# Performance work log

Hardware: AMD Instinct MI355X
Metric: run time of the kernel (lower is better)

Reference implementation:

```python
import jax, jax.numpy as jnp
import numpy as np

FIRE_RATE = 0.5
ANGLE = 0.0


def _kernels(angle):
    dx = np.outer([1, 2, 1], [-1, 0, 1]) / 8.0
    dy = dx.T
    dlap = np.array([[1, 2, 1], [2, -12, 2], [1, 2, 1]]) / 8.0
    dlap2 = np.array([[0, 1, 0], [1, -4, 1], [0, 1, 0]]) / 8.0
    c = np.cos(angle * np.pi / 180.0)
    s = np.sin(angle * np.pi / 180.0)
    w1 = c * dx - s * dy
    w2 = s * dx + c * dy
    return [jnp.asarray(k, jnp.float32) for k in (w1, w2, dlap, dlap2)]


def _dwconv(x, k):
    # x: [B,H,W,C], k: [3,3] applied depthwise (same kernel every channel)
    C = x.shape[-1]
    rhs = jnp.broadcast_to(k[:, :, None, None], (3, 3, 1, C))
    return jax.lax.conv_general_dilated(
        x, rhs, window_strides=(1, 1), padding='SAME',
        dimension_numbers=('NHWC', 'HWIO', 'NHWC'), feature_group_count=C)


def _alive(x):
    # 3x3 max-pool (stride 1, SAME) over alpha channel (index 3) > 0.1
    a = jax.lax.reduce_window(x[..., 3:4], -jnp.inf, jax.lax.max,
                              (1, 3, 3, 1), (1, 1, 1, 1), 'SAME')
    return a > 0.1


def _update(x, W0, b0, W1, key):
    pre_life = _alive(x)                                  # [B,H,W,1] bool
    ks = _kernels(ANGLE)
    y = jnp.concatenate([x] + [_dwconv(x, k) for k in ks], axis=-1)  # [B,H,W,5C]
    h = jax.nn.relu(y @ W0 + b0)                          # [B,H,W,hidden]
    d = h @ W1                                            # [B,H,W,C]
    stoch = (jax.random.uniform(key, d.shape[:3] + (1,)) > FIRE_RATE).astype(d.dtype)
    x = x + d * stoch
    life = (pre_life & _alive(x)).astype(x.dtype)
    return x * life


def setup_inputs() -> dict:
    key = jax.random.key(0)
    k1, k2, k3, k4 = jax.random.split(key, 4)
    B, H, W, C, HID = 8, 256, 256, 16, 128
    return {
        'x': jax.random.normal(k1, (B, H, W, C), jnp.float32),
        'W0': jax.random.normal(k2, (5 * C, HID), jnp.float32) * 0.05,
        'b0': jax.random.normal(k3, (HID,), jnp.float32) * 0.05,
        'W1': jax.random.normal(k4, (HID, C), jnp.float32) * 0.05,
        'steps': 2,
    }


def reference(x, W0, b0, W1, steps):
    base = jax.random.key(42)
    for step in range(steps):
        x = _update(x, W0, b0, W1, jax.random.fold_in(base, step))
    return x
```

## Files before the change

### kernel.cpp

```cpp
#include <hip/hip_runtime.h>
#include <stdint.h>

#define BB 8
#define HH 256
#define WW 256
#define CC 16
#define HID 128
#define NPIX (BB*HH*WW)
#define MTILE 64
#define NBLK (NPIX/MTILE)

typedef _Float16 h8 __attribute__((ext_vector_type(8)));
typedef __fp16   fp16v2 __attribute__((ext_vector_type(2)));
typedef float    f4 __attribute__((ext_vector_type(4)));

#define YPK_HI     0
#define YPK_MID    3328
#define ALPHA5_OFF 6656
#define LIFE_OFF   6996
#define LDS_DW     8192

__host__ __device__ __forceinline__ uint32_t rotl32(uint32_t x, int r) {
  return (x << r) | (x >> (32 - r));
}

__host__ __device__ inline void threefry2x32(uint32_t k0, uint32_t k1,
                                             uint32_t x0, uint32_t x1,
                                             uint32_t& o0, uint32_t& o1) {
  const uint32_t ks2 = k0 ^ k1 ^ 0x1BD11BDAu;
  x0 += k0; x1 += k1;
#define TF_R4(a,b,c,d) \
  x0 += x1; x1 = rotl32(x1,(a)); x1 ^= x0; \
  x0 += x1; x1 = rotl32(x1,(b)); x1 ^= x0; \
  x0 += x1; x1 = rotl32(x1,(c)); x1 ^= x0; \
  x0 += x1; x1 = rotl32(x1,(d)); x1 ^= x0;
  TF_R4(13,15,26,6)   x0 += k1;  x1 += ks2 + 1u;
  TF_R4(17,29,16,24)  x0 += ks2; x1 += k0 + 2u;
  TF_R4(13,15,26,6)   x0 += k0;  x1 += k1 + 3u;
  TF_R4(17,29,16,24)  x0 += k1;  x1 += ks2 + 4u;
  TF_R4(13,15,26,6)   x0 += ks2; x1 += k0 + 5u;
#undef TF_R4
  o0 = x0; o1 = x1;
}

__device__ __forceinline__ void split2(float a, float b, uint32_t& hi, uint32_t& mid) {
  _Float16 ha = (_Float16)a, hb = (_Float16)b;
  union { _Float16 h[2]; uint32_t u; } ph;
  ph.h[0] = ha; ph.h[1] = hb; hi = ph.u;
  float ra = a - (float)ha, rb = b - (float)hb;
  union { fp16v2 h; uint32_t u; } pu;
  pu.h = __builtin_amdgcn_cvt_pkrtz(ra, rb);
  mid = pu.u;
}

__global__ __launch_bounds__(256)
void prep_frags(const float* __restrict__ W0g, const float* __restrict__ W1g,
                uint32_t* __restrict__ W0F, uint32_t* __restrict__ W1F) {
  const int tid = blockIdx.x * 256 + threadIdx.x;
  for (int idx = tid; idx < 6144; idx += gridDim.x * 256) {
    const int r = idx & 3, l = (idx >> 2) & 63, ks = (idx >> 8) % 3, n = idx / 768;
    const int g = l >> 4, c = l & 15;
    const int k0 = 32 * ks + 8 * g + 2 * r;
    const int hid = 16 * n + c;
    const float a = (k0     < 80) ? W0g[k0 * HID + hid]       : 0.f;
    const float b = (k0 + 1 < 80) ? W0g[(k0 + 1) * HID + hid] : 0.f;
    uint32_t hi, mid; split2(a, b, hi, mid);
    W0F[(size_t)(((n * 3 + ks) * 2 + 0) * 64 + l) * 4 + r] = hi;
    W0F[(size_t)(((n * 3 + ks) * 2 + 1) * 64 + l) * 4 + r] = mid;
  }
  for (int idx = tid; idx < 1024; idx += gridDim.x * 256) {
    const int r = idx & 3, l = (idx >> 2) & 63, ks = idx >> 8;
    const int g = l >> 4, c = l & 15;
    float va[2];
#pragma unroll
    for (int h = 0; h < 2; ++h) {
      const int khat = 2 * g + 16 * (r & 1) + 8 * h + (r >> 1);
      va[h] = W1g[(size_t)(32 * ks + khat) * CC + c];
    }
    uint32_t hi, mid; split2(va[0], va[1], hi, mid);
    W1F[(size_t)((ks * 2 + 0) * 64 + l) * 4 + r] = hi;
    W1F[(size_t)((ks * 2 + 1) * 64 + l) * 4 + r] = mid;
  }
}

template <int APPLY_LIFE>
__global__ __launch_bounds__(256, 5)
void step_fused(const float* __restrict__ xin,
                const uint32_t* __restrict__ W0F,
                const uint32_t* __restrict__ W1F,
                const float* __restrict__ b0g,
                const float* __restrict__ aPrev,
                const unsigned char* __restrict__ mPrev,
                float* __restrict__ xn,
                float* __restrict__ alpha_out,
                unsigned char* __restrict__ prelife,
                uint32_t k0, uint32_t k1) {
  __shared__ uint32_t LDSU[LDS_DW];
  float* const LDSF = (float*)LDSU;

  const int t    = threadIdx.x;
  const int blk  = blockIdx.x;
  const int lane = t & 63;
  const int w    = __builtin_amdgcn_readfirstlane(t >> 6);
  const int g    = lane >> 4;
  const int c15  = lane & 15;

  uint4 BH[2][2], BM[2][2];
#pragma unroll
  for (int nl = 0; nl < 2; ++nl) {
    const int n = 2 * w + nl;
    BH[0][nl] = *(const uint4*)(W0F + (size_t)(((n * 3 + 0) * 2 + 0) * 64 + lane) * 4);
    BM[0][nl] = *(const uint4*)(W0F + (size_t)(((n * 3 + 0) * 2 + 1) * 64 + lane) * 4);
  }
  const float bv0 = b0g[16 * (2 * w + 0) + c15];
  const float bv1 = b0g[16 * (2 * w + 1) + c15];

  const int base_ = blk * MTILE;
  const int bi    = base_ >> 16;
  const int rc    = base_ & 0xFFFF;
  const int ic    = rc >> 8;
  const int jc0   = rc & 0xFF;

  if constexpr (APPLY_LIFE) {
    const float* ap = aPrev + (size_t)bi * (HH * WW);
    for (int it = t; it < 340; it += 256) {
      const int r = it / 68, c = it - r * 68;
      const int ii = ic - 2 + r, jj = jc0 - 2 + c;
      float v = 0.f;
      if ((unsigned)ii < (unsigned)HH && (unsigned)jj < (unsigned)WW)
        v = ap[ii * WW + jj];
      LDSF[ALPHA5_OFF + it] = v;
    }
    __syncthreads();
    if (t < 198) {
      const int r = t / 66, xx = t - r * 66;
      const float* a0 = &LDSF[ALPHA5_OFF + r * 68 + xx];
      const float m0 = fmaxf(fmaxf(a0[0],   a0[1]),   a0[2]);
      const float m1 = fmaxf(fmaxf(a0[68],  a0[69]),  a0[70]);
      const float m2 = fmaxf(fmaxf(a0[136], a0[137]), a0[138]);
      const float mm = fmaxf(fmaxf(m0, m1), m2);
      const int ii = ic - 1 + r, jj = jc0 - 1 + xx;
      int pl = 0;
      if ((unsigned)ii < (unsigned)HH && (unsigned)jj < (unsigned)WW)
        pl = mPrev[(size_t)bi * (HH * WW) + ii * WW + jj];
      LDSF[LIFE_OFF + t] = (pl && mm > 0.1f) ? 1.0f : 0.0f;
    }
    __syncthreads();
  }

  const int px  = 16 * w + c15;
  const int c4  = 4 * g;
  const int gpx = base_ + px;
  const int jc  = jc0 + px;

  const float DXW[3][3] = {{-0.125f, 0.0f, 0.125f},
                           {-0.25f,  0.0f, 0.25f },
                           {-0.125f, 0.0f, 0.125f}};
  const float DYW[3][3] = {{-0.125f, -0.25f, -0.125f},
                           { 0.0f,    0.0f,   0.0f  },
                           { 0.125f,  0.25f,  0.125f}};
  const float LPW[3][3] = {{0.125f, 0.25f, 0.125f},
                           {0.25f, -1.5f,  0.25f },
                           {0.125f, 0.25f, 0.125f}};
  const float L2W[3][3] = {{0.0f,   0.125f, 0.0f  },
                           {0.125f, -0.5f,  0.125f},
                           {0.0f,   0.125f, 0.0f  }};

  float ctr[4] = {0,0,0,0};
  float adx[4] = {0,0,0,0};
  float ady[4] = {0,0,0,0};
  float alp[4] = {0,0,0,0};
  float al2[4] = {0,0,0,0};
  float amax = 0.0f;

  const float* xb = xin + (size_t)bi * (HH * WW * CC);
#pragma unroll
  for (int di = -1; di <= 1; ++di) {
#pragma unroll
    for (int dj = -1; dj <= 1; ++dj) {
      const int ii = ic + di, jj = jc + dj;
      const bool ok = ((unsigned)ii < (unsigned)HH) && ((unsigned)jj < (unsigned)WW);
      float4 p = make_float4(0.f, 0.f, 0.f, 0.f);
      if (ok) p = *(const float4*)(xb + ((size_t)(ii * WW + jj) * CC + c4));
      if constexpr (APPLY_LIFE) {
        const float lf = LDSF[LIFE_OFF + (di + 1) * 66 + (px + dj + 1)];
        p.x *= lf; p.y *= lf; p.z *= lf; p.w *= lf;
      }
      const float wdx = DXW[di+1][dj+1], wdy = DYW[di+1][dj+1];
      const float wlp = LPW[di+1][dj+1], wl2 = L2W[di+1][dj+1];
      const float pv[4] = {p.x, p.y, p.z, p.w};
#pragma unroll
      for (int q = 0; q < 4; ++q) {
        if (di == 0 && dj == 0) ctr[q] = pv[q];
        if (wdx != 0.f) adx[q] = fmaf(pv[q], wdx, adx[q]);
        if (wdy != 0.f) ady[q] = fmaf(pv[q], wdy, ady[q]);
        if (wlp != 0.f) alp[q] = fmaf(pv[q], wlp, alp[q]);
        if (wl2 != 0.f) al2[q] = fmaf(pv[q], wl2, al2[q]);
      }
      if (g == 0) amax = fmaxf(amax, p.w);
    }
  }

  float fire01;
  {
    uint32_t lo, hi2;
    threefry2x32(k0, k1, 0u, (uint32_t)gpx, lo, hi2);
    const uint32_t bits = lo ^ hi2;
    const float u = __uint_as_float((bits >> 9) | 0x3f800000u) - 1.0f;
    fire01 = (u > 0.5f) ? 1.0f : 0.0f;
  }

  {
    const int q2 = g << 1;
#define WRYPK(grp, A) do { \
    uint32_t h0_, m0_, h1_, m1_; \
    split2(A[0], A[1], h0_, m0_); split2(A[2], A[3], h1_, m1_); \
    const int kk_ = 8 * (grp) + q2; \
    *(uint2*)&LDSU[YPK_HI  + px * 52 + kk_] = make_uint2(h0_, h1_); \
    *(uint2*)&LDSU[YPK_MID + px * 52 + kk_] = make_uint2(m0_, m1_); \
  } while (0)
    WRYPK(0, ctr); WRYPK(1, adx); WRYPK(2, ady); WRYPK(3, alp); WRYPK(4, al2);
#undef WRYPK
  }
#pragma unroll
  for (int j = 0; j < 4; ++j) {
    const int pos = t * 4 + j;
    const int plane = pos >> 9, rem = pos & 511;
    LDSU[plane * 3328 + (rem >> 3) * 52 + 40 + (rem & 7)] = 0u;
  }
  if (g == 0) prelife[gpx] = (amax > 0.1f) ? 1 : 0;

  __syncthreads();

  f4 C1[4][2];
#pragma unroll
  for (int m = 0; m < 4; ++m) {
    C1[m][0] = (f4){bv0, bv0, bv0, bv0};
    C1[m][1] = (f4){bv1, bv1, bv1, bv1};
  }

#define LOADB(par, kss) do { \
  _Pragma("unroll") for (int nl_ = 0; nl_ < 2; ++nl_) { \
    const int n_ = 2 * w + nl_; \
    BH[par][nl_] = *(const uint4*)(W0F + (size_t)(((n_ * 3 + (kss)) * 2 + 0) * 64 + lane) * 4); \
    BM[par][nl_] = *(const uint4*)(W0F + (size_t)(((n_ * 3 + (kss)) * 2 + 1) * 64 + lane) * 4); \
  } } while (0)

  const int abase = c15 * 52 + 4 * g;
#pragma unroll
  for (int ks = 0; ks < 3; ++ks) {
    if (ks == 0) LOADB(1, 1);
    if (ks == 1) LOADB(0, 2);
    const int cur = ks & 1;
#pragma unroll
    for (int m = 0; m < 4; ++m) {
      const uint4 uh = *(const uint4*)&LDSU[YPK_HI  + abase + m * 832 + 16 * ks];
      const uint4 um = *(const uint4*)&LDSU[YPK_MID + abase + m * 832 + 16 * ks];
      const h8 ah = __builtin_bit_cast(h8, uh);
      const h8 am = __builtin_bit_cast(h8, um);
#pragma unroll
      for (int nl = 0; nl < 2; ++nl) {
        const h8 bh = __builtin_bit_cast(h8, BH[cur][nl]);
        const h8 bm = __builtin_bit_cast(h8, BM[cur][nl]);
        C1[m][nl] = __builtin_amdgcn_mfma_f32_16x16x32_f16(ah, bh, C1[m][nl], 0, 0, 0);
        C1[m][nl] = __builtin_amdgcn_mfma_f32_16x16x32_f16(am, bh, C1[m][nl], 0, 0, 0);
        C1[m][nl] = __builtin_amdgcn_mfma_f32_16x16x32_f16(ah, bm, C1[m][nl], 0, 0, 0);
      }
    }
  }
#undef LOADB

  __syncthreads();

  {
    const int sg = (g & 1) << 4;
    const int hid0 = 32 * w + c15;
    const int hid1 = hid0 + 16;
    const int hx00 = hid0 ^ sg,       hx01 = hid0 ^ (sg | 1);
    const int hx02 = hid0 ^ (sg | 8), hx03 = hid0 ^ (sg | 9);
    const int hx10 = hid1 ^ sg,       hx11 = hid1 ^ (sg | 1);
    const int hx12 = hid1 ^ (sg | 8), hx13 = hid1 ^ (sg | 9);
#pragma unroll
    for (int m = 0; m < 4; ++m) {
      const int rowb = (16 * m + 4 * g) * 128;
      {
        f4 hv = C1[m][0];
        LDSF[rowb +   0 + hx00] = fmaxf(hv.x, 0.f);
        LDSF[rowb + 128 + hx01] = fmaxf(hv.y, 0.f);
        LDSF[rowb + 256 + hx02] = fmaxf(hv.z, 0.f);
        LDSF[rowb + 384 + hx03] = fmaxf(hv.w, 0.f);
      }
      {
        f4 hv = C1[m][1];
        LDSF[rowb +   0 + hx10] = fmaxf(hv.x, 0.f);
        LDSF[rowb + 128 + hx11] = fmaxf(hv.y, 0.f);
        LDSF[rowb + 256 + hx12] = fmaxf(hv.z, 0.f);
        LDSF[rowb + 384 + hx13] = fmaxf(hv.w, 0.f);
      }
    }
  }

  uint4 W1H[4], W1M[4];
#pragma unroll
  for (int ks = 0; ks < 4; ++ks) {
    W1H[ks] = *(const uint4*)(W1F + (size_t)((ks * 2 + 0) * 64 + lane) * 4);
    W1M[ks] = *(const uint4*)(W1F + (size_t)((ks * 2 + 1) * 64 + lane) * 4);
  }

  __syncthreads();

  f4 C2 = (f4){0.f, 0.f, 0.f, 0.f};
  {
    const int swzr  = (c15 & 1) | ((c15 & 6) << 2);
    const int hbase = px * 128 + 2 * g;
    int ka[4], kb[4];
#pragma unroll
    for (int r = 0; r < 4; ++r) {
      const int K0 = 16 * (r & 1) + (r >> 1);
      ka[r] = K0 ^ swzr;
      kb[r] = (K0 + 8) ^ swzr;
    }
#pragma unroll
    for (int ks = 0; ks < 4; ++ks) {
      uint32_t ph[4], pm[4];
#pragma unroll
      for (int r = 0; r < 4; ++r) {
        const float a = LDSF[hbase + 32 * ks + ka[r]];
        const float b = LDSF[hbase + 32 * ks + kb[r]];
        split2(a, b, ph[r], pm[r]);
      }
      const uint4 uh = make_uint4(ph[0], ph[1], ph[2], ph[3]);
      const uint4 um = make_uint4(pm[0], pm[1], pm[2], pm[3]);
      const h8 bh = __builtin_bit_cast(h8, uh);
      const h8 bm = __builtin_bit_cast(h8, um);
      const h8 ah = __builtin_bit_cast(h8, W1H[ks]);
      const h8 am = __builtin_bit_cast(h8, W1M[ks]);
      C2 = __builtin_amdgcn_mfma_f32_16x16x32_f16(ah, bh, C2, 0, 0, 0);
      C2 = __builtin_amdgcn_mfma_f32_16x16x32_f16(am, bh, C2, 0, 0, 0);
      C2 = __builtin_amdgcn_mfma_f32_16x16x32_f16(ah, bm, C2, 0, 0, 0);
    }
  }

  {
    f4 xv;
    xv.x = fmaf(C2.x, fire01, ctr[0]);
    xv.y = fmaf(C2.y, fire01, ctr[1]);
    xv.z = fmaf(C2.z, fire01, ctr[2]);
    xv.w = fmaf(C2.w, fire01, ctr[3]);
    *(f4*)&xn[(size_t)gpx * CC + c4] = xv;
    if (g == 0) alpha_out[gpx] = xv.w;
  }
}

__global__ __launch_bounds__(256)
void life_final(float* __restrict__ out,
                const float* __restrict__ alpha,
                const unsigned char* __restrict__ prelife) {
  const int idx = blockIdx.x * 256 + threadIdx.x;
  const int b  = idx >> 16;
  const int ij = idx & 0xFFFF;
  const int i  = ij >> 8;
  const int j  = ij & 0xFF;

  const float* ab = alpha + (size_t)b * (HH * WW);
  float amax = 0.0f;
#pragma unroll
  for (int di = -1; di <= 1; ++di) {
    const int ii = i + di;
    if ((unsigned)ii >= (unsigned)HH) continue;
#pragma unroll
    for (int dj = -1; dj <= 1; ++dj) {
      const int jj = j + dj;
      if ((unsigned)jj >= (unsigned)WW) continue;
      amax = fmaxf(amax, ab[(size_t)ii * WW + jj]);
    }
  }
  const bool life = (prelife[idx] != 0) && (amax > 0.1f);
  if (!life) {
    const float4 z = make_float4(0.0f, 0.0f, 0.0f, 0.0f);
    float4* dst = (float4*)(out + (size_t)idx * CC);
    dst[0] = z; dst[1] = z; dst[2] = z; dst[3] = z;
  }
}

extern "C" void kernel_launch(void* const* d_in, const int* in_sizes, int n_in,
                              void* d_out, int out_size, void* d_ws, size_t ws_size,
                              hipStream_t stream) {
  (void)in_sizes; (void)n_in; (void)out_size; (void)ws_size;
  const float* x  = (const float*)d_in[0];
  const float* W0 = (const float*)d_in[1];
  const float* b0 = (const float*)d_in[2];
  const float* W1 = (const float*)d_in[3];
  float* out = (float*)d_out;

  float* xn = (float*)d_ws;
  float* alphaA = xn + (size_t)NPIX * CC;
  float* alphaB = alphaA + NPIX;
  unsigned char* maskA = (unsigned char*)(alphaB + NPIX);
  unsigned char* maskB = maskA + NPIX;
  uint32_t* W0F = (uint32_t*)(maskB + NPIX);
  uint32_t* W1F = W0F + 12288;

  prep_frags<<<24, 256, 0, stream>>>(W0, W1, W0F, W1F);

  uint32_t fk0, fk1;
  threefry2x32(0u, 42u, 0u, 0u, fk0, fk1);
  step_fused<0><<<NBLK, 256, 0, stream>>>(x, W0F, W1F, b0, nullptr, nullptr,
                                          xn, alphaA, maskA, fk0, fk1);
  threefry2x32(0u, 42u, 0u, 1u, fk0, fk1);
  step_fused<1><<<NBLK, 256, 0, stream>>>(xn, W0F, W1F, b0, alphaA, maskA,
                                          out, alphaB, maskB, fk0, fk1);
  life_final<<<NPIX / 256, 256, 0, stream>>>(out, alphaB, maskB);
}
```

Measured before the change: 222.7 us.

## Fold depthwise stencils into W0 and feed raw 3x3 patches to MFMA

The four fixed 3x3 depthwise kernels and the identity channel are folded into the first layer's weights on the device, producing an effective 144x128 weight over the raw 3x3 neighbourhood. The main kernel now stages a 3x66 halo of the input into LDS once per block as split fp16 hi/mid values and feeds the 9 taps directly to the MFMAs. This replaces per-thread 9-tap global gathers and scalar stencil FMAs. In exchange, K grows from 96 to 160, so each block issues more MFMAs. The folded weights also change the rounding of the hi/mid split.

```diff
diff --git a/kernel.cpp b/kernel.cpp
--- a/kernel.cpp
+++ b/kernel.cpp
@@ -14,10 +14,12 @@
 typedef __fp16   fp16v2 __attribute__((ext_vector_type(2)));
 typedef float    f4 __attribute__((ext_vector_type(4)));
 
-#define YPK_HI     0
-#define YPK_MID    3328
-#define ALPHA5_OFF 6656
-#define LIFE_OFF   6996
+#define XH_OFF     0
+#define XM_OFF     2112
+#define ALF_OFF    4224
+#define ALPHA5_OFF 4424
+#define LIFE_OFF   4764
+#define HS_OFF     0
 #define LDS_DW     8192
 
 __host__ __device__ __forceinline__ uint32_t rotl32(uint32_t x, int r) {
@@ -56,17 +58,33 @@
 __global__ __launch_bounds__(256)
 void prep_frags(const float* __restrict__ W0g, const float* __restrict__ W1g,
                 uint32_t* __restrict__ W0F, uint32_t* __restrict__ W1F) {
+  const float KW[5][9] = {
+    {0.f,0.f,0.f, 0.f,1.f,0.f, 0.f,0.f,0.f},
+    {-0.125f,0.f,0.125f, -0.25f,0.f,0.25f, -0.125f,0.f,0.125f},
+    {-0.125f,-0.25f,-0.125f, 0.f,0.f,0.f, 0.125f,0.25f,0.125f},
+    {0.125f,0.25f,0.125f, 0.25f,-1.5f,0.25f, 0.125f,0.25f,0.125f},
+    {0.f,0.125f,0.f, 0.125f,-0.5f,0.125f, 0.f,0.125f,0.f}};
   const int tid = blockIdx.x * 256 + threadIdx.x;
-  for (int idx = tid; idx < 6144; idx += gridDim.x * 256) {
-    const int r = idx & 3, l = (idx >> 2) & 63, ks = (idx >> 8) % 3, n = idx / 768;
+  for (int idx = tid; idx < 10240; idx += gridDim.x * 256) {
+    const int r = idx & 3, l = (idx >> 2) & 63;
+    const int ks = (idx >> 8) % 5, n = (idx >> 8) / 5;
     const int g = l >> 4, c = l & 15;
-    const int k0 = 32 * ks + 8 * g + 2 * r;
     const int hid = 16 * n + c;
-    const float a = (k0     < 80) ? W0g[k0 * HID + hid]       : 0.f;
-    const float b = (k0 + 1 < 80) ? W0g[(k0 + 1) * HID + hid] : 0.f;
-    uint32_t hi, mid; split2(a, b, hi, mid);
-    W0F[(size_t)(((n * 3 + ks) * 2 + 0) * 64 + l) * 4 + r] = hi;
-    W0F[(size_t)(((n * 3 + ks) * 2 + 1) * 64 + l) * 4 + r] = mid;
+    float v[2];
+#pragma unroll
+    for (int h = 0; h < 2; ++h) {
+      const int k = 32 * ks + 8 * g + 2 * r + h;
+      float acc = 0.f;
+      if (k < 144) {
+        const int tap = k >> 4, ch = k & 15;
+        for (int grp = 0; grp < 5; ++grp)
+          acc += KW[grp][tap] * W0g[(16 * grp + ch) * HID + hid];
+      }
+      v[h] = acc;
+    }
+    uint32_t hi, mid; split2(v[0], v[1], hi, mid);
+    W0F[(size_t)(((n * 5 + ks) * 2 + 0) * 64 + l) * 4 + r] = hi;
+    W0F[(size_t)(((n * 5 + ks) * 2 + 1) * 64 + l) * 4 + r] = mid;
   }
   for (int idx = tid; idx < 1024; idx += gridDim.x * 256) {
     const int r = idx & 3, l = (idx >> 2) & 63, ks = idx >> 8;
@@ -106,12 +124,13 @@
   const int c15  = lane & 15;
 
   uint4 BH[2][2], BM[2][2];
-#pragma unroll
-  for (int nl = 0; nl < 2; ++nl) {
-    const int n = 2 * w + nl;
-    BH[0][nl] = *(const uint4*)(W0F + (size_t)(((n * 3 + 0) * 2 + 0) * 64 + lane) * 4);
-    BM[0][nl] = *(const uint4*)(W0F + (size_t)(((n * 3 + 0) * 2 + 1) * 64 + lane) * 4);
-  }
+#define LOADB(buf, kss) do { \
+  _Pragma("unroll") for (int nl_ = 0; nl_ < 2; ++nl_) { \
+    const int n_ = 2 * w + nl_; \
+    BH[buf][nl_] = *(const uint4*)(W0F + (size_t)(((n_ * 5 + (kss)) * 2 + 0) * 64 + lane) * 4); \
+    BM[buf][nl_] = *(const uint4*)(W0F + (size_t)(((n_ * 5 + (kss)) * 2 + 1) * 64 + lane) * 4); \
+  } } while (0)
+  LOADB(0, 0);
   const float bv0 = b0g[16 * (2 * w + 0) + c15];
   const float bv1 = b0g[16 * (2 * w + 1) + c15];
 
@@ -120,6 +139,8 @@
   const int rc    = base_ & 0xFFFF;
   const int ic    = rc >> 8;
   const int jc0   = rc & 0xFF;
+
+  const float* xb = xin + (size_t)bi * (HH * WW * CC);
 
   if constexpr (APPLY_LIFE) {
     const float* ap = aPrev + (size_t)bi * (HH * WW);
@@ -148,59 +169,39 @@
     __syncthreads();
   }
 
+  for (int s = t; s < 792; s += 256) {
+    const int site = s >> 2, q = s & 3;
+    const int row = site / 66, cc = site - row * 66;
+    const int ii = ic - 1 + row, jj = jc0 - 1 + cc;
+    float4 p = make_float4(0.f, 0.f, 0.f, 0.f);
+    if ((unsigned)ii < (unsigned)HH && (unsigned)jj < (unsigned)WW)
+      p = *(const float4*)(xb + ((size_t)(ii * WW + jj) * CC + 4 * q));
+    if constexpr (APPLY_LIFE) {
+      const float lf = LDSF[LIFE_OFF + row * 66 + cc];
+      p.x *= lf; p.y *= lf; p.z *= lf; p.w *= lf;
+    }
+    uint32_t h0, m0, h1, m1;
+    split2(p.x, p.y, h0, m0);
+    split2(p.z, p.w, h1, m1);
+    const int dst = row * 528 + cc * 8 + q * 2;
+    *(uint2*)&LDSU[XH_OFF + dst] = make_uint2(h0, h1);
+    *(uint2*)&LDSU[XM_OFF + dst] = make_uint2(m0, m1);
+    if (q == 0) LDSF[ALF_OFF + row * 66 + cc] = p.w;
+  }
+  for (int z = t; z < 1056; z += 256) {
+    const int pl = (z >= 528) ? 1 : 0;
+    LDSU[(pl ? XM_OFF : XH_OFF) + 1584 + (z - pl * 528)] = 0u;
+  }
+
   const int px  = 16 * w + c15;
   const int c4  = 4 * g;
   const int gpx = base_ + px;
   const int jc  = jc0 + px;
-
-  const float DXW[3][3] = {{-0.125f, 0.0f, 0.125f},
-                           {-0.25f,  0.0f, 0.25f },
-                           {-0.125f, 0.0f, 0.125f}};
-  const float DYW[3][3] = {{-0.125f, -0.25f, -0.125f},
-                           { 0.0f,    0.0f,   0.0f  },
-                           { 0.125f,  0.25f,  0.125f}};
-  const float LPW[3][3] = {{0.125f, 0.25f, 0.125f},
-                           {0.25f, -1.5f,  0.25f },
-                           {0.125f, 0.25f, 0.125f}};
-  const float L2W[3][3] = {{0.0f,   0.125f, 0.0f  },
-                           {0.125f, -0.5f,  0.125f},
-                           {0.0f,   0.125f, 0.0f  }};
-
-  float ctr[4] = {0,0,0,0};
-  float adx[4] = {0,0,0,0};
-  float ady[4] = {0,0,0,0};
-  float alp[4] = {0,0,0,0};
-  float al2[4] = {0,0,0,0};
-  float amax = 0.0f;
-
-  const float* xb = xin + (size_t)bi * (HH * WW * CC);
-#pragma unroll
-  for (int di = -1; di <= 1; ++di) {
-#pragma unroll
-    for (int dj = -1; dj <= 1; ++dj) {
-      const int ii = ic + di, jj = jc + dj;
-      const bool ok = ((unsigned)ii < (unsigned)HH) && ((unsigned)jj < (unsigned)WW);
-      float4 p = make_float4(0.f, 0.f, 0.f, 0.f);
-      if (ok) p = *(const float4*)(xb + ((size_t)(ii * WW + jj) * CC + c4));
-      if constexpr (APPLY_LIFE) {
-        const float lf = LDSF[LIFE_OFF + (di + 1) * 66 + (px + dj + 1)];
-        p.x *= lf; p.y *= lf; p.z *= lf; p.w *= lf;
-      }
-      const float wdx = DXW[di+1][dj+1], wdy = DYW[di+1][dj+1];
-      const float wlp = LPW[di+1][dj+1], wl2 = L2W[di+1][dj+1];
-      const float pv[4] = {p.x, p.y, p.z, p.w};
-#pragma unroll
-      for (int q = 0; q < 4; ++q) {
-        if (di == 0 && dj == 0) ctr[q] = pv[q];
-        if (wdx != 0.f) adx[q] = fmaf(pv[q], wdx, adx[q]);
-        if (wdy != 0.f) ady[q] = fmaf(pv[q], wdy, ady[q]);
-        if (wlp != 0.f) alp[q] = fmaf(pv[q], wlp, alp[q]);
-        if (wl2 != 0.f) al2[q] = fmaf(pv[q], wl2, al2[q]);
-      }
-      if (g == 0) amax = fmaxf(amax, p.w);
-    }
-  }
-
+  f4 ctr4 = *(const f4*)(xb + ((size_t)(ic * WW + jc) * CC + c4));
+  if constexpr (APPLY_LIFE) {
+    const float lf = LDSF[LIFE_OFF + 66 + (px + 1)];
+    ctr4.x *= lf; ctr4.y *= lf; ctr4.z *= lf; ctr4.w *= lf;
+  }
   float fire01;
   {
     uint32_t lo, hi2;
@@ -210,27 +211,25 @@
     fire01 = (u > 0.5f) ? 1.0f : 0.0f;
   }
 
+  __syncthreads();
+
   {
-    const int q2 = g << 1;
-#define WRYPK(grp, A) do { \
-    uint32_t h0_, m0_, h1_, m1_; \
-    split2(A[0], A[1], h0_, m0_); split2(A[2], A[3], h1_, m1_); \
-    const int kk_ = 8 * (grp) + q2; \
-    *(uint2*)&LDSU[YPK_HI  + px * 52 + kk_] = make_uint2(h0_, h1_); \
-    *(uint2*)&LDSU[YPK_MID + px * 52 + kk_] = make_uint2(m0_, m1_); \
-  } while (0)
-    WRYPK(0, ctr); WRYPK(1, adx); WRYPK(2, ady); WRYPK(3, alp); WRYPK(4, al2);
-#undef WRYPK
-  }
-#pragma unroll
-  for (int j = 0; j < 4; ++j) {
-    const int pos = t * 4 + j;
-    const int plane = pos >> 9, rem = pos & 511;
-    LDSU[plane * 3328 + (rem >> 3) * 52 + 40 + (rem & 7)] = 0u;
-  }
-  if (g == 0) prelife[gpx] = (amax > 0.1f) ? 1 : 0;
-
-  __syncthreads();
+    float am = 0.f;
+#pragma unroll
+    for (int r = 0; r < 3; ++r) {
+      const float* a0 = &LDSF[ALF_OFF + r * 66 + px];
+      am = fmaxf(am, fmaxf(fmaxf(a0[0], a0[1]), a0[2]));
+    }
+    if (g == 0) prelife[gpx] = (am > 0.1f) ? 1 : 0;
+  }
+
+  const int gh  = (lane >> 5) & 1;
+  const int com = c15 * 8 + ((lane >> 4) & 1) * 4;
+  const int aoff0 = com + (gh ? 8    : 0);
+  const int aoff1 = com + (gh ? 528  : 16);
+  const int aoff2 = com + (gh ? 544  : 536);
+  const int aoff3 = com + (gh ? 1064 : 1056);
+  const int aoff4 = com + (gh ? 1584 : 1072);
 
   f4 C1[4][2];
 #pragma unroll
@@ -239,35 +238,31 @@
     C1[m][1] = (f4){bv1, bv1, bv1, bv1};
   }
 
-#define LOADB(par, kss) do { \
-  _Pragma("unroll") for (int nl_ = 0; nl_ < 2; ++nl_) { \
-    const int n_ = 2 * w + nl_; \
-    BH[par][nl_] = *(const uint4*)(W0F + (size_t)(((n_ * 3 + (kss)) * 2 + 0) * 64 + lane) * 4); \
-    BM[par][nl_] = *(const uint4*)(W0F + (size_t)(((n_ * 3 + (kss)) * 2 + 1) * 64 + lane) * 4); \
+#define G1SLAB(aoffk, buf) do { \
+  _Pragma("unroll") for (int m = 0; m < 4; ++m) { \
+    const uint4 uh = *(const uint4*)&LDSU[XH_OFF + (aoffk) + 128 * m]; \
+    const uint4 um = *(const uint4*)&LDSU[XM_OFF + (aoffk) + 128 * m]; \
+    const h8 ah = __builtin_bit_cast(h8, uh); \
+    const h8 am = __builtin_bit_cast(h8, um); \
+    _Pragma("unroll") for (int nl = 0; nl < 2; ++nl) { \
+      const h8 bh = __builtin_bit_cast(h8, BH[buf][nl]); \
+      const h8 bm = __builtin_bit_cast(h8, BM[buf][nl]); \
+      C1[m][nl] = __builtin_amdgcn_mfma_f32_16x16x32_f16(ah, bh, C1[m][nl], 0, 0, 0); \
+      C1[m][nl] = __builtin_amdgcn_mfma_f32_16x16x32_f16(am, bh, C1[m][nl], 0, 0, 0); \
+      C1[m][nl] = __builtin_amdgcn_mfma_f32_16x16x32_f16(ah, bm, C1[m][nl], 0, 0, 0); \
+    } \
   } } while (0)
 
-  const int abase = c15 * 52 + 4 * g;
-#pragma unroll
-  for (int ks = 0; ks < 3; ++ks) {
-    if (ks == 0) LOADB(1, 1);
-    if (ks == 1) LOADB(0, 2);
-    const int cur = ks & 1;
-#pragma unroll
-    for (int m = 0; m < 4; ++m) {
-      const uint4 uh = *(const uint4*)&LDSU[YPK_HI  + abase + m * 832 + 16 * ks];
-      const uint4 um = *(const uint4*)&LDSU[YPK_MID + abase + m * 832 + 16 * ks];
-      const h8 ah = __builtin_bit_cast(h8, uh);
-      const h8 am = __builtin_bit_cast(h8, um);
-#pragma unroll
-      for (int nl = 0; nl < 2; ++nl) {
-        const h8 bh = __builtin_bit_cast(h8, BH[cur][nl]);
-        const h8 bm = __builtin_bit_cast(h8, BM[cur][nl]);
-        C1[m][nl] = __builtin_amdgcn_mfma_f32_16x16x32_f16(ah, bh, C1[m][nl], 0, 0, 0);
-        C1[m][nl] = __builtin_amdgcn_mfma_f32_16x16x32_f16(am, bh, C1[m][nl], 0, 0, 0);
-        C1[m][nl] = __builtin_amdgcn_mfma_f32_16x16x32_f16(ah, bm, C1[m][nl], 0, 0, 0);
-      }
-    }
-  }
+  LOADB(1, 1);
+  G1SLAB(aoff0, 0);
+  LOADB(0, 2);
+  G1SLAB(aoff1, 1);
+  LOADB(1, 3);
+  G1SLAB(aoff2, 0);
+  LOADB(0, 4);
+  G1SLAB(aoff3, 1);
+  G1SLAB(aoff4, 0);
+#undef G1SLAB
 #undef LOADB
 
   __syncthreads();
@@ -343,10 +338,10 @@
 
   {
     f4 xv;
-    xv.x = fmaf(C2.x, fire01, ctr[0]);
-    xv.y = fmaf(C2.y, fire01, ctr[1]);
-    xv.z = fmaf(C2.z, fire01, ctr[2]);
-    xv.w = fmaf(C2.w, fire01, ctr[3]);
+    xv.x = fmaf(C2.x, fire01, ctr4.x);
+    xv.y = fmaf(C2.y, fire01, ctr4.y);
+    xv.z = fmaf(C2.z, fire01, ctr4.z);
+    xv.w = fmaf(C2.w, fire01, ctr4.w);
     *(f4*)&xn[(size_t)gpx * CC + c4] = xv;
     if (g == 0) alpha_out[gpx] = xv.w;
   }
@@ -399,9 +394,9 @@
   unsigned char* maskA = (unsigned char*)(alphaB + NPIX);
   unsigned char* maskB = maskA + NPIX;
   uint32_t* W0F = (uint32_t*)(maskB + NPIX);
-  uint32_t* W1F = W0F + 12288;
-
-  prep_frags<<<24, 256, 0, stream>>>(W0, W1, W0F, W1F);
+  uint32_t* W1F = W0F + 20480;
+
+  prep_frags<<<40, 256, 0, stream>>>(W0, W1, W0F, W1F);
 
   uint32_t fk0, fk1;
   threefry2x32(0u, 42u, 0u, 0u, fk0, fk1);
```

Result: slower. 249.1 us (+11.9%).
